# Optimization experiments

Measured on AMD Instinct MI355X. Metric: run time of the kernel, lower is better.

## Reference

```python
import jax, jax.numpy as jnp
from jax import lax
import numpy as np

B, P, N = 4, 12000, 100   # batch, max_pillars, max_points_per_pillar
H, W = 108, 124           # pseudo-image size from forward()
DN = ('NCHW', 'HWIO', 'NCHW')


def _conv(x, k, b):
    y = lax.conv_general_dilated(x, k, (1, 1), 'SAME', dimension_numbers=DN)
    return y + b[None, :, None, None]


def _cbr(x, k, b, s, t):
    # Conv2d + folded BatchNorm2d (eval: per-channel scale/shift) + ReLU
    y = _conv(x, k, b)
    return jax.nn.relu(y * s[None, :, None, None] + t[None, :, None, None])


def _pool(x):
    return lax.reduce_window(x, -jnp.inf, lax.max, (1, 1, 2, 2), (1, 1, 2, 2), 'VALID')


def setup_inputs() -> dict:
    key = jax.random.key(0)
    ks = iter(jax.random.split(key, 64))
    d = {}
    d['pillars'] = jax.random.normal(next(ks), (B, P, N, 9), jnp.float32)

    def w(shape, scale=0.05):
        return jax.random.normal(next(ks), shape, jnp.float32) * scale

    d['w1'] = w((9, 64)); d['b1'] = w((64,))
    d['s1'] = 1.0 + w((64,)); d['t1'] = w((64,))
    d['w2'] = w((64, 64)); d['b2'] = w((64,))
    d['s2'] = 1.0 + w((64,)); d['t2'] = w((64,))
    chans = [(64, 64), (64, 64), (64, 128), (128, 128), (128, 256), (256, 256)]
    for i, (ci, co) in enumerate(chans, 1):
        d['ck%d' % i] = w((3, 3, ci, co)); d['cb%d' % i] = w((co,))
        d['cs%d' % i] = 1.0 + w((co,)); d['ct%d' % i] = w((co,))
    d['hk1'] = w((3, 3, 256, 256)); d['hb1'] = w((256,))
    d['hk2'] = w((1, 1, 256, 10)); d['hb2'] = w((10,))
    d['num_points'] = jax.random.randint(next(ks), (B, P), 0, 100, jnp.int32)
    return d


def reference(pillars, w1, b1, s1, t1, w2, b2, s2, t2,
              ck1, cb1, cs1, ct1, ck2, cb2, cs2, ct2,
              ck3, cb3, cs3, ct3, ck4, cb4, cs4, ct4,
              ck5, cb5, cs5, ct5, ck6, cb6, cs6, ct6,
              hk1, hb1, hk2, hb2, num_points):
    # pillar feature net: Linear+BN(folded)+ReLU x2, batched over all points  [B,P,N,9] -> [B,P,N,64]
    h = jax.nn.relu((pillars @ w1 + b1) * s1 + t1)
    h = jax.nn.relu((h @ w2 + b2) * s2 + t2)
    # masked segment-max over the variable-length point groups
    mask = jnp.arange(N)[None, None, :] < num_points[:, :, None]          # [B,P,N]
    neg = jnp.finfo(h.dtype).min
    feat = jnp.max(jnp.where(mask[..., None], h, neg), axis=2)            # [B,P,64]
    valid = num_points > 0
    feat = jnp.where(valid[..., None], feat, 0.0)
    cnt = jnp.maximum(jnp.sum(valid, axis=1), 1).astype(feat.dtype)       # [B]
    mean = jnp.sum(feat, axis=1) / cnt[:, None]                           # [B,64]
    # nearest-interpolate a 1x1 map to HxW == broadcast
    x = jnp.broadcast_to(mean[:, :, None, None], (pillars.shape[0], 64, H, W))
    # 2D backbone
    x = _cbr(x, ck1, cb1, cs1, ct1); x = _cbr(x, ck2, cb2, cs2, ct2); x = _pool(x)
    x = _cbr(x, ck3, cb3, cs3, ct3); x = _cbr(x, ck4, cb4, cs4, ct4); x = _pool(x)
    x = _cbr(x, ck5, cb5, cs5, ct5); x = _cbr(x, ck6, cb6, cs6, ct6)
    # detection head
    y = jax.nn.relu(_conv(x, hk1, hb1))
    return _conv(y, hk2, hb2)   # [B, num_classes+7=10, 27, 31]
```

## Files before the change

### kernel.cpp

```cpp
#include <hip/hip_runtime.h>

typedef __bf16 vbf8 __attribute__((ext_vector_type(8)));
typedef __bf16 vbf4 __attribute__((ext_vector_type(4)));
typedef unsigned short us8 __attribute__((ext_vector_type(8)));
typedef float f32x4 __attribute__((ext_vector_type(4)));
typedef float f32x4u __attribute__((ext_vector_type(4), aligned(4)));

__global__ void setup_kernel(const float* __restrict__ w1, const float* __restrict__ b1,
                             const float* __restrict__ s1, const float* __restrict__ t1,
                             const float* __restrict__ w2, const float* __restrict__ b2,
                             const float* __restrict__ s2, const float* __restrict__ t2,
                             __bf16* __restrict__ wfrag, float4* __restrict__ cfrag) {
  int l = threadIdx.x;
  int s = l & 15, g = l >> 4;
#pragma unroll
  for (int n = 0; n < 4; ++n) {
    int co = s + 16 * n;
#pragma unroll
    for (int e = 0; e < 8; ++e) {
      int k = g * 8 + e;
      wfrag[(n * 64 + l) * 8 + e] = (k < 9) ? (__bf16)w1[k * 64 + co] : (__bf16)0.f;
      wfrag[((4 + n) * 64 + l) * 8 + e] = (__bf16)w2[k * 64 + co];
      wfrag[((8 + n) * 64 + l) * 8 + e] = (__bf16)w2[(32 + k) * 64 + co];
    }
    cfrag[n * 64 + l] = make_float4(s1[co], fmaf(b1[co], s1[co], t1[co]),
                                    s2[co], fmaf(b2[co], s2[co], t2[co]));
  }
}

__global__ void convw_kernel(const float* __restrict__ k1, const float* __restrict__ k2,
                             const float* __restrict__ k3, const float* __restrict__ k4,
                             const float* __restrict__ k5, const float* __restrict__ k6,
                             const float* __restrict__ kh, __bf16* __restrict__ wT) {
  int id = blockIdx.x * 256 + threadIdx.x;
  if (id >= 1769472) return;
  const float* src; int CI, CO, base;
  if (id < 36864)        { src = k1; base = 0;       CI = 64;  CO = 64; }
  else if (id < 73728)   { src = k2; base = 36864;   CI = 64;  CO = 64; }
  else if (id < 147456)  { src = k3; base = 73728;   CI = 64;  CO = 128; }
  else if (id < 294912)  { src = k4; base = 147456;  CI = 128; CO = 128; }
  else if (id < 589824)  { src = k5; base = 294912;  CI = 128; CO = 256; }
  else if (id < 1179648) { src = k6; base = 589824;  CI = 256; CO = 256; }
  else                   { src = kh; base = 1179648; CI = 256; CO = 256; }
  int loc = id - base;
  int tap = loc / (CI * CO); int rem = loc % (CI * CO);
  int co = rem / CI; int ci = rem % CI;
  wT[id] = (__bf16)src[(tap * CI + ci) * CO + co];
}

__global__ void zero_borders_kernel(__bf16* __restrict__ a64, __bf16* __restrict__ b64,
                                    __bf16* __restrict__ c128a, __bf16* __restrict__ c128b,
                                    __bf16* __restrict__ c256a, __bf16* __restrict__ c256b) {
  int idx = blockIdx.x * 256 + threadIdx.x;
  __bf16* buf; int H2, C, p;
  if (idx < 34848)       { buf = (idx < 17424) ? a64 : b64;     H2 = 66; C = 64;  p = idx % 17424; }
  else if (idx < 44096)  { int q = idx - 34848; buf = (q < 4624) ? c128a : c128b; H2 = 34; C = 128; p = q % 4624; }
  else if (idx < 46688)  { int q = idx - 44096; buf = (q < 1296) ? c256a : c256b; H2 = 18; C = 256; p = q % 1296; }
  else return;
  int w = p % H2; int h = (p / H2) % H2;
  if (h != 0 && h != H2 - 1 && w != 0 && w != H2 - 1) return;
  us8 zz = {0, 0, 0, 0, 0, 0, 0, 0};
  __bf16* q = buf + (size_t)p * C;
  for (int c = 0; c < C; c += 8) *(us8*)(q + c) = zz;
}

__global__ __launch_bounds__(256) void pillar_kernel(
    const float* __restrict__ pil, const int* __restrict__ npt,
    const __bf16* __restrict__ wfrag, const float4* __restrict__ cfrag,
    float* __restrict__ partial, int* __restrict__ pcnt)
{
  __shared__ __bf16 ldsa[4][16 * 80];
  __shared__ float redf[4][64];
  __shared__ int redc[4];
  const int tid = threadIdx.x;
  const int wv = tid >> 6, lane = tid & 63;
  const int s = lane & 15, g = lane >> 4;
  __bf16* lds = ldsa[wv];
  const int wid = blockIdx.x * 4 + wv;
  const int b = wid / 6000;
  const int p0 = (wid - b * 6000) * 2;

  vbf8 w1f[4], w2f0[4], w2f1[4];
  float a1[4], be1[4], a2[4], be2[4];
#pragma unroll
  for (int n = 0; n < 4; ++n) {
    w1f[n]  = *(const vbf8*)(wfrag + ((0 + n) * 64 + lane) * 8);
    w2f0[n] = *(const vbf8*)(wfrag + ((4 + n) * 64 + lane) * 8);
    w2f1[n] = *(const vbf8*)(wfrag + ((8 + n) * 64 + lane) * 8);
    float4 c = cfrag[n * 64 + lane];
    a1[n] = c.x; be1[n] = c.y; a2[n] = c.z; be2[n] = c.w;
  }

  float fsum[4] = {0.f, 0.f, 0.f, 0.f};
  int cnt = 0;

  for (int i = 0; i < 2; ++i) {
    int pidx = b * 12000 + p0 + i;
    int np = npt[pidx];
    if (np <= 0) continue;
    ++cnt;
    float feat[4][4];
#pragma unroll
    for (int n = 0; n < 4; ++n)
#pragma unroll
      for (int r = 0; r < 4; ++r) feat[n][r] = 0.f;

    int ngrp = (np + 15) >> 4;
    const float* pbase = pil + (size_t)pidx * 900;
    for (int grp = 0; grp < ngrp; ++grp) {
      int pt = grp * 16 + s; pt = min(pt, 99);
      const float* ptp = pbase + pt * 9;
      f32x4u lo = *(const f32x4u*)ptp;
      f32x4u hi = *(const f32x4u*)(ptp + 4);
      float v8 = ptp[8];
      vbf8 af;
      af[0] = (__bf16)(g == 0 ? lo[0] : (g == 1 ? v8 : 0.f));
      af[1] = (__bf16)(g == 0 ? lo[1] : 0.f);
      af[2] = (__bf16)(g == 0 ? lo[2] : 0.f);
      af[3] = (__bf16)(g == 0 ? lo[3] : 0.f);
      af[4] = (__bf16)(g == 0 ? hi[0] : 0.f);
      af[5] = (__bf16)(g == 0 ? hi[1] : 0.f);
      af[6] = (__bf16)(g == 0 ? hi[2] : 0.f);
      af[7] = (__bf16)(g == 0 ? hi[3] : 0.f);

      const f32x4 z = {0.f, 0.f, 0.f, 0.f};
      f32x4 d1[4];
#pragma unroll
      for (int n = 0; n < 4; ++n)
        d1[n] = __builtin_amdgcn_mfma_f32_16x16x32_bf16(af, w1f[n], z, 0, 0, 0);

#pragma unroll
      for (int n = 0; n < 4; ++n)
#pragma unroll
        for (int r = 0; r < 4; ++r) {
          float h = fmaxf(fmaf(d1[n][r], a1[n], be1[n]), 0.f);
          int pt2 = g * 4 + r;
          int ch = (s + 16 * n) ^ ((pt2 >> 2) << 3);
          lds[pt2 * 80 + ch] = (__bf16)h;
        }
      __builtin_amdgcn_wave_barrier();

      vbf8 a2f0 = *(const vbf8*)(lds + s * 80 + ((g * 8) ^ ((s >> 2) << 3)));
      vbf8 a2f1 = *(const vbf8*)(lds + s * 80 + ((32 + g * 8) ^ ((s >> 2) << 3)));
      f32x4 d2[4];
#pragma unroll
      for (int n = 0; n < 4; ++n) {
        d2[n] = __builtin_amdgcn_mfma_f32_16x16x32_bf16(a2f0, w2f0[n], z, 0, 0, 0);
        d2[n] = __builtin_amdgcn_mfma_f32_16x16x32_bf16(a2f1, w2f1[n], d2[n], 0, 0, 0);
      }
#pragma unroll
      for (int n = 0; n < 4; ++n)
#pragma unroll
        for (int r = 0; r < 4; ++r) {
          float h = fmaxf(fmaf(d2[n][r], a2[n], be2[n]), 0.f);
          if (grp * 16 + g * 4 + r < np) feat[n][r] = fmaxf(feat[n][r], h);
        }
    }
#pragma unroll
    for (int n = 0; n < 4; ++n) {
      float m = fmaxf(fmaxf(feat[n][0], feat[n][1]), fmaxf(feat[n][2], feat[n][3]));
      m = fmaxf(m, __shfl_xor(m, 16));
      m = fmaxf(m, __shfl_xor(m, 32));
      fsum[n] += m;
    }
  }
  if (g == 0) {
#pragma unroll
    for (int n = 0; n < 4; ++n) redf[wv][s + 16 * n] = fsum[n];
  }
  if (lane == 0) redc[wv] = cnt;
  __syncthreads();
  if (tid < 64) {
    float tot = redf[0][tid] + redf[1][tid] + redf[2][tid] + redf[3][tid];
    partial[blockIdx.x * 64 + tid] = tot;
    if (tid == 0) pcnt[blockIdx.x] = redc[0] + redc[1] + redc[2] + redc[3];
  }
}

__global__ void mean_kernel(const float* __restrict__ partial,
                            const int* __restrict__ pcnt,
                            float* __restrict__ mean) {
  int b = blockIdx.x, t = threadIdx.x;
  int c = t & 63, q = t >> 6;
  float sum = 0.f;
  for (int w = q; w < 1500; w += 4) sum += partial[(b * 1500 + w) * 64 + c];
  int cl = 0;
  for (int w = t; w < 1500; w += 256) cl += pcnt[b * 1500 + w];
  __shared__ float sh[256];
  __shared__ int shc[256];
  sh[t] = sum; shc[t] = cl;
  __syncthreads();
  for (int o = 128; o > 0; o >>= 1) {
    if (t < o) shc[t] += shc[t + o];
    __syncthreads();
  }
  if (t < 64) {
    float tot = sh[t] + sh[t + 64] + sh[t + 128] + sh[t + 192];
    mean[b * 64 + t] = tot / (float)(shc[0] > 0 ? shc[0] : 1);
  }
}

__global__ void broadcast_kernel(const float* __restrict__ mean,
                                 __bf16* __restrict__ x0) {
  int idx = blockIdx.x * 256 + threadIdx.x;
  int c8 = idx & 7; int rest = idx >> 3;
  int w = rest & 63; rest >>= 6;
  int h = rest & 63; int b = rest >> 6;
  const float* mb = mean + b * 64 + c8 * 8;
  vbf8 v;
#pragma unroll
  for (int e = 0; e < 8; ++e) v[e] = (__bf16)mb[e];
  *(vbf8*)(x0 + (((size_t)(b * 66 + h + 1) * 66) + (w + 1)) * 64 + c8 * 8) = v;
}

template <int CIN, int COUT, int HW>
__global__ __launch_bounds__(256) void kconv_kernel(
    const __bf16* __restrict__ x, const __bf16* __restrict__ wt,
    float* __restrict__ kpart)
{
  constexpr int H2 = HW + 2;
  constexpr int NT = COUT / 64;
  constexpr int KC = CIN / 32;
  constexpr int MTOT = 4 * HW * HW;
  constexpr int LOG = (HW == 64) ? 6 : (HW == 32) ? 5 : 4;
  const int tid = threadIdx.x, wv = tid >> 6, lane = tid & 63;
  const int s = lane & 15, g = lane >> 4;
  const int task = blockIdx.x * 4 + wv;
  const int kg = task % 3;
  const int t2 = task / 3;
  const int nt = t2 % NT;
  const int mt = t2 / NT;
  const int m0 = mt * 32;
  const int b = m0 >> (2 * LOG);
  const int mb = m0 - (b << (2 * LOG));

  size_t arow[2];
#pragma unroll
  for (int mf = 0; mf < 2; ++mf) {
    int m = mb + mf * 16 + s;
    int hh = m >> LOG, ww = m & (HW - 1);
    arow[mf] = ((size_t)(b * H2 + hh) * H2 + ww) * CIN;
  }

  f32x4 acc[2][4];
#pragma unroll
  for (int mf = 0; mf < 2; ++mf)
#pragma unroll
    for (int nf = 0; nf < 4; ++nf) acc[mf][nf] = (f32x4){0.f, 0.f, 0.f, 0.f};

#pragma unroll
  for (int j = 0; j < 3; ++j) {
    const int tap = kg * 3 + j;
    const int dh = tap / 3, dw = tap % 3;
    const size_t aoff = ((size_t)dh * H2 + dw) * CIN + 8 * g;
    const __bf16* wtap = wt + ((size_t)tap * COUT + nt * 64) * CIN + 8 * g;
#pragma unroll 2
    for (int ck = 0; ck < KC; ++ck) {
      vbf8 a0 = *(const vbf8*)(x + arow[0] + aoff + ck * 32);
      vbf8 a1 = *(const vbf8*)(x + arow[1] + aoff + ck * 32);
#pragma unroll
      for (int nf = 0; nf < 4; ++nf) {
        vbf8 bb = *(const vbf8*)(wtap + (size_t)(nf * 16 + s) * CIN + ck * 32);
        acc[0][nf] = __builtin_amdgcn_mfma_f32_16x16x32_bf16(a0, bb, acc[0][nf], 0, 0, 0);
        acc[1][nf] = __builtin_amdgcn_mfma_f32_16x16x32_bf16(a1, bb, acc[1][nf], 0, 0, 0);
      }
    }
  }

  float* kp = kpart + (size_t)kg * MTOT * COUT;
#pragma unroll
  for (int mf = 0; mf < 2; ++mf)
#pragma unroll
    for (int nf = 0; nf < 4; ++nf) {
      int co = nt * 64 + nf * 16 + s;
#pragma unroll
      for (int r = 0; r < 4; ++r) {
        int m = m0 + mf * 16 + 4 * g + r;
        kp[(size_t)m * COUT + co] = acc[mf][nf][r];
      }
    }
}

template <int COUT, int HW, bool HAS_BN, bool OUT_F32>
__global__ __launch_bounds__(256) void reduce_kernel(
    const float* __restrict__ kpart, const float* __restrict__ cb,
    const float* __restrict__ cs, const float* __restrict__ ct,
    __bf16* __restrict__ ypad, float* __restrict__ yf32)
{
  constexpr int H2 = HW + 2;
  constexpr int MTOT = 4 * HW * HW;
  constexpr int CQ = COUT / 4;
  constexpr int LOG = (HW == 64) ? 6 : (HW == 32) ? 5 : 4;
  int idx = blockIdx.x * 256 + threadIdx.x;
  int cq = idx % CQ; int m = idx / CQ;
  int co0 = cq * 4;
  const f32x4* f4 = (const f32x4*)kpart;
  f32x4 v = f4[(size_t)m * CQ + cq];
  f32x4 v1 = f4[((size_t)MTOT + m) * CQ + cq];
  f32x4 v2 = f4[((size_t)2 * MTOT + m) * CQ + cq];
  v += v1 + v2;
  f32x4 r;
  if (HAS_BN) {
    f32x4 sc = *(const f32x4*)(cs + co0);
    f32x4 bb = *(const f32x4*)(cb + co0);
    f32x4 tt = *(const f32x4*)(ct + co0);
#pragma unroll
    for (int e = 0; e < 4; ++e) r[e] = fmaxf(fmaf(v[e], sc[e], fmaf(bb[e], sc[e], tt[e])), 0.f);
  } else {
    f32x4 bb = *(const f32x4*)(cb + co0);
#pragma unroll
    for (int e = 0; e < 4; ++e) r[e] = fmaxf(v[e] + bb[e], 0.f);
  }
  if constexpr (OUT_F32) {
    *(f32x4*)(yf32 + (size_t)m * COUT + co0) = r;
  } else {
    int b = m >> (2 * LOG);
    int mm = m - (b << (2 * LOG));
    int hh = mm >> LOG, ww = mm & (HW - 1);
    vbf4 o;
#pragma unroll
    for (int e = 0; e < 4; ++e) o[e] = (__bf16)r[e];
    *(vbf4*)(ypad + (((size_t)(b * H2 + hh + 1) * H2) + ww + 1) * COUT + co0) = o;
  }
}

template <int C, int HI>
__global__ void pool_kernel(const __bf16* __restrict__ x, __bf16* __restrict__ y) {
  constexpr int HO = HI / 2, W2I = HI + 2, W2O = HO + 2, C8 = C / 8;
  int idx = blockIdx.x * 256 + threadIdx.x;
  if (idx >= 4 * W2O * W2O * C8) return;
  int c8 = idx % C8; int rest = idx / C8;
  int wo = rest % W2O; rest /= W2O;
  int ho = rest % W2O; int b = rest / W2O;
  us8 out;
  if (ho == 0 || ho == W2O - 1 || wo == 0 || wo == W2O - 1) {
    out = (us8){0, 0, 0, 0, 0, 0, 0, 0};
  } else {
    int hi = 2 * (ho - 1) + 1, wi = 2 * (wo - 1) + 1;
    const unsigned short* p =
        (const unsigned short*)x + (((size_t)(b * W2I + hi) * W2I) + wi) * C + c8 * 8;
    us8 v0 = *(const us8*)p;
    us8 v1 = *(const us8*)(p + C);
    us8 v2 = *(const us8*)(p + (size_t)W2I * C);
    us8 v3 = *(const us8*)(p + (size_t)W2I * C + C);
#pragma unroll
    for (int e = 0; e < 8; ++e) {
      unsigned short a = v0[e] > v1[e] ? v0[e] : v1[e];
      unsigned short c = v2[e] > v3[e] ? v2[e] : v3[e];
      out[e] = a > c ? a : c;
    }
  }
  *(us8*)((unsigned short*)y + (((size_t)(b * W2O + ho) * W2O) + wo) * C + c8 * 8) = out;
}

__global__ void head2_kernel(const float* __restrict__ x, const float* __restrict__ wk,
                             const float* __restrict__ bias, float* __restrict__ y) {
  int h = blockIdx.x, b = blockIdx.y;
  int t = threadIdx.x;
  int co = t & 15, w = t >> 4;
  if (co >= 10) return;
  const float* xr = x + ((size_t)(b * 16 + h) * 16 + w) * 256;
  float acc = 0.f;
#pragma unroll 4
  for (int ci = 0; ci < 256; ci += 4) {
    float4 in4 = *(const float4*)(xr + ci);
    acc = fmaf(in4.x, wk[(ci + 0) * 10 + co], acc);
    acc = fmaf(in4.y, wk[(ci + 1) * 10 + co], acc);
    acc = fmaf(in4.z, wk[(ci + 2) * 10 + co], acc);
    acc = fmaf(in4.w, wk[(ci + 3) * 10 + co], acc);
  }
  y[((size_t)(b * 16 + h) * 16 + w) * 10 + co] = acc + bias[co];
}

__global__ void scatter_kernel(const float* __restrict__ y, float* __restrict__ out) {
  int idx = blockIdx.x * 256 + threadIdx.x;
  if (idx >= 4 * 10 * 27 * 31) return;
  int c = idx % 31;
  int r = (idx / 31) % 27;
  int ch = (idx / (31 * 27)) % 10;
  int b = idx / (31 * 27 * 10);
  int rr = (r <= 7) ? r : ((r >= 20) ? r - 11 : 7);
  int cc = (c <= 7) ? c : ((c >= 24) ? c - 15 : 7);
  out[idx] = y[((size_t)(b * 16 + rr) * 16 + cc) * 10 + ch];
}

extern "C" void kernel_launch(void* const* d_in, const int* in_sizes, int n_in,
                              void* d_out, int out_size, void* d_ws, size_t ws_size,
                              hipStream_t stream) {
  (void)in_sizes; (void)n_in; (void)out_size; (void)ws_size;
  const float* pillars = (const float*)d_in[0];
  const float* w1 = (const float*)d_in[1];
  const float* b1 = (const float*)d_in[2];
  const float* s1 = (const float*)d_in[3];
  const float* t1 = (const float*)d_in[4];
  const float* w2 = (const float*)d_in[5];
  const float* b2 = (const float*)d_in[6];
  const float* s2 = (const float*)d_in[7];
  const float* t2 = (const float*)d_in[8];
  const float* ck[6], *cbv[6], *csv[6], *ctv[6];
  for (int i = 0; i < 6; ++i) {
    ck[i]  = (const float*)d_in[9 + i * 4];
    cbv[i] = (const float*)d_in[10 + i * 4];
    csv[i] = (const float*)d_in[11 + i * 4];
    ctv[i] = (const float*)d_in[12 + i * 4];
  }
  const float* hk1 = (const float*)d_in[33];
  const float* hb1 = (const float*)d_in[34];
  const float* hk2 = (const float*)d_in[35];
  const float* hb2 = (const float*)d_in[36];
  const int* num_points = (const int*)d_in[37];
  float* out = (float*)d_out;

  char* wsb = (char*)d_ws;
  size_t off = 0;
  auto alloc = [&](size_t n) { char* p = wsb + off; off = (off + n + 255) & ~(size_t)255; return p; };
  float*  kpart  = (float*)alloc(12582912);
  float*  ppart  = (float*)alloc(1536000);
  int*    pcnt   = (int*)alloc(24000);
  float*  mean   = (float*)alloc(1024);
  __bf16* wfrag  = (__bf16*)alloc(12288);
  float4* cfrag  = (float4*)alloc(4096);
  float*  h2out  = (float*)alloc(40960);
  __bf16* wT     = (__bf16*)alloc(3538944);
  __bf16* A64    = (__bf16*)alloc(2230272);
  __bf16* B64    = (__bf16*)alloc(2230272);
  __bf16* PL64   = (__bf16*)alloc(591872);
  __bf16* C128A  = (__bf16*)alloc(1183744);
  __bf16* C128B  = (__bf16*)alloc(1183744);
  __bf16* PL128  = (__bf16*)alloc(331776);
  __bf16* C256A  = (__bf16*)alloc(663552);
  __bf16* C256B  = (__bf16*)alloc(663552);
  float*  h1out  = (float*)alloc(1048576);

  __bf16* wt1 = wT + 0;       __bf16* wt2 = wT + 36864;
  __bf16* wt3 = wT + 73728;   __bf16* wt4 = wT + 147456;
  __bf16* wt5 = wT + 294912;  __bf16* wt6 = wT + 589824;
  __bf16* wth = wT + 1179648;

  setup_kernel<<<1, 64, 0, stream>>>(w1, b1, s1, t1, w2, b2, s2, t2, wfrag, cfrag);
  convw_kernel<<<6912, 256, 0, stream>>>(ck[0], ck[1], ck[2], ck[3], ck[4], ck[5],
                                         hk1, wT);
  zero_borders_kernel<<<183, 256, 0, stream>>>(A64, B64, C128A, C128B, C256A, C256B);

  pillar_kernel<<<6000, 256, 0, stream>>>(pillars, num_points, wfrag, cfrag,
                                          ppart, pcnt);
  mean_kernel<<<4, 256, 0, stream>>>(ppart, pcnt, mean);
  broadcast_kernel<<<512, 256, 0, stream>>>(mean, A64);

  kconv_kernel<64, 64, 64><<<384, 256, 0, stream>>>(A64, wt1, kpart);
  reduce_kernel<64, 64, true, false><<<1024, 256, 0, stream>>>(
      kpart, cbv[0], csv[0], ctv[0], B64, nullptr);
  kconv_kernel<64, 64, 64><<<384, 256, 0, stream>>>(B64, wt2, kpart);
  reduce_kernel<64, 64, true, false><<<1024, 256, 0, stream>>>(
      kpart, cbv[1], csv[1], ctv[1], A64, nullptr);
  pool_kernel<64, 64><<<145, 256, 0, stream>>>(A64, PL64);
  kconv_kernel<64, 128, 32><<<192, 256, 0, stream>>>(PL64, wt3, kpart);
  reduce_kernel<128, 32, true, false><<<512, 256, 0, stream>>>(
      kpart, cbv[2], csv[2], ctv[2], C128A, nullptr);
  kconv_kernel<128, 128, 32><<<192, 256, 0, stream>>>(C128A, wt4, kpart);
  reduce_kernel<128, 32, true, false><<<512, 256, 0, stream>>>(
      kpart, cbv[3], csv[3], ctv[3], C128B, nullptr);
  pool_kernel<128, 32><<<81, 256, 0, stream>>>(C128B, PL128);
  kconv_kernel<128, 256, 16><<<96, 256, 0, stream>>>(PL128, wt5, kpart);
  reduce_kernel<256, 16, true, false><<<256, 256, 0, stream>>>(
      kpart, cbv[4], csv[4], ctv[4], C256A, nullptr);
  kconv_kernel<256, 256, 16><<<96, 256, 0, stream>>>(C256A, wt6, kpart);
  reduce_kernel<256, 16, true, false><<<256, 256, 0, stream>>>(
      kpart, cbv[5], csv[5], ctv[5], C256B, nullptr);
  kconv_kernel<256, 256, 16><<<96, 256, 0, stream>>>(C256B, wth, kpart);
  reduce_kernel<256, 16, false, true><<<256, 256, 0, stream>>>(
      kpart, hb1, nullptr, nullptr, nullptr, h1out);

  head2_kernel<<<dim3(16, 4), 256, 0, stream>>>(h1out, hk2, hb2, h2out);
  scatter_kernel<<<131, 256, 0, stream>>>(h2out, out);
}
```

Baseline: 372.3 us.

## Fold BN into pillar MLP weights, keep layer-1 output in registers, tile weight transpose

The first-layer MFMA is transposed so its output lands directly in the A-fragment layout for the second layer, removing the LDS round-trip and wave barrier. BatchNorm scale is folded into the bf16 weights, and the layer-1 bias rides as an extra K column of constant 1. The layer-2 shift is fed as the MFMA accumulator init. Full groups skip the per-point mask, and the conv-weight transpose now goes through a shared-memory tile for coalesced accesses. The cost is slightly different bf16 rounding from folding the scales into the weights.

Result: faster. 340.8 us (-8.5%).

```diff
diff --git a/kernel.cpp b/kernel.cpp
--- a/kernel.cpp
+++ b/kernel.cpp
@@ -10,42 +10,64 @@
                              const float* __restrict__ s1, const float* __restrict__ t1,
                              const float* __restrict__ w2, const float* __restrict__ b2,
                              const float* __restrict__ s2, const float* __restrict__ t2,
-                             __bf16* __restrict__ wfrag, float4* __restrict__ cfrag) {
+                             __bf16* __restrict__ wfrag, float* __restrict__ be2f) {
   int l = threadIdx.x;
   int s = l & 15, g = l >> 4;
 #pragma unroll
-  for (int n = 0; n < 4; ++n) {
-    int co = s + 16 * n;
+  for (int m = 0; m < 4; ++m) {
+    int c = 32 * (m & 1) + 8 * (s >> 2) + 4 * (m >> 1) + (s & 3);
 #pragma unroll
     for (int e = 0; e < 8; ++e) {
       int k = g * 8 + e;
-      wfrag[(n * 64 + l) * 8 + e] = (k < 9) ? (__bf16)w1[k * 64 + co] : (__bf16)0.f;
-      wfrag[((4 + n) * 64 + l) * 8 + e] = (__bf16)w2[k * 64 + co];
-      wfrag[((8 + n) * 64 + l) * 8 + e] = (__bf16)w2[(32 + k) * 64 + co];
-    }
-    cfrag[n * 64 + l] = make_float4(s1[co], fmaf(b1[co], s1[co], t1[co]),
-                                    s2[co], fmaf(b2[co], s2[co], t2[co]));
-  }
-}
-
-__global__ void convw_kernel(const float* __restrict__ k1, const float* __restrict__ k2,
-                             const float* __restrict__ k3, const float* __restrict__ k4,
-                             const float* __restrict__ k5, const float* __restrict__ k6,
-                             const float* __restrict__ kh, __bf16* __restrict__ wT) {
-  int id = blockIdx.x * 256 + threadIdx.x;
-  if (id >= 1769472) return;
-  const float* src; int CI, CO, base;
-  if (id < 36864)        { src = k1; base = 0;       CI = 64;  CO = 64; }
-  else if (id < 73728)   { src = k2; base = 36864;   CI = 64;  CO = 64; }
-  else if (id < 147456)  { src = k3; base = 73728;   CI = 64;  CO = 128; }
-  else if (id < 294912)  { src = k4; base = 147456;  CI = 128; CO = 128; }
-  else if (id < 589824)  { src = k5; base = 294912;  CI = 128; CO = 256; }
-  else if (id < 1179648) { src = k6; base = 589824;  CI = 256; CO = 256; }
-  else                   { src = kh; base = 1179648; CI = 256; CO = 256; }
-  int loc = id - base;
-  int tap = loc / (CI * CO); int rem = loc % (CI * CO);
-  int co = rem / CI; int ci = rem % CI;
-  wT[id] = (__bf16)src[(tap * CI + ci) * CO + co];
+      float v = 0.f;
+      if (k < 9)       v = w1[k * 64 + c] * s1[c];
+      else if (k == 9) v = fmaf(b1[c], s1[c], t1[c]);
+      wfrag[(m * 64 + l) * 8 + e] = (__bf16)v;
+    }
+    int co = s + 16 * m;
+#pragma unroll
+    for (int e = 0; e < 8; ++e) {
+      int k = g * 8 + e;
+      wfrag[((4 + m) * 64 + l) * 8 + e] = (__bf16)(w2[k * 64 + co] * s2[co]);
+      wfrag[((8 + m) * 64 + l) * 8 + e] = (__bf16)(w2[(32 + k) * 64 + co] * s2[co]);
+    }
+    be2f[m * 64 + l] = fmaf(b2[co], s2[co], t2[co]);
+  }
+}
+
+__global__ __launch_bounds__(256) void convw_kernel(
+    const float* __restrict__ k1, const float* __restrict__ k2,
+    const float* __restrict__ k3, const float* __restrict__ k4,
+    const float* __restrict__ k5, const float* __restrict__ k6,
+    const float* __restrict__ kh, __bf16* __restrict__ wT) {
+  __shared__ float tile[64][65];
+  const int tCI[7]    = {64, 64, 64, 128, 128, 256, 256};
+  const int tCO[7]    = {64, 64, 128, 128, 256, 256, 256};
+  const int tOFF[7]   = {0, 36864, 73728, 147456, 294912, 589824, 1179648};
+  const int tTILES[7] = {9, 9, 18, 36, 72, 144, 144};
+  int bid = blockIdx.x;
+  int ti = 0, acc = 0;
+  while (ti < 6 && bid >= acc + tTILES[ti]) { acc += tTILES[ti]; ++ti; }
+  int lt = bid - acc;
+  int CI = tCI[ti], CO = tCO[ti];
+  const float* src;
+  if (ti == 0) src = k1; else if (ti == 1) src = k2; else if (ti == 2) src = k3;
+  else if (ti == 3) src = k4; else if (ti == 4) src = k5; else if (ti == 5) src = k6;
+  else src = kh;
+  int cot = CO / 64, tpt = (CI / 64) * cot;
+  int tap = lt / tpt; int r2 = lt - tap * tpt;
+  int ci0 = (r2 / cot) * 64, co0 = (r2 % cot) * 64;
+  const float* sp = src + (size_t)(tap * CI + ci0) * CO + co0;
+  int t = threadIdx.x;
+  int lr = t >> 6, lc = t & 63;
+#pragma unroll
+  for (int rr = 0; rr < 64; rr += 4)
+    tile[rr + lr][lc] = sp[(size_t)(rr + lr) * CO + lc];
+  __syncthreads();
+  __bf16* dst = wT + tOFF[ti] + ((size_t)tap * CO + co0) * CI + ci0;
+#pragma unroll
+  for (int rr = 0; rr < 64; rr += 4)
+    dst[(size_t)(rr + lr) * CI + lc] = (__bf16)tile[lc][rr + lr];
 }
 
 __global__ void zero_borders_kernel(__bf16* __restrict__ a64, __bf16* __restrict__ b64,
@@ -66,29 +88,26 @@
 
 __global__ __launch_bounds__(256) void pillar_kernel(
     const float* __restrict__ pil, const int* __restrict__ npt,
-    const __bf16* __restrict__ wfrag, const float4* __restrict__ cfrag,
+    const __bf16* __restrict__ wfrag, const float* __restrict__ be2f,
     float* __restrict__ partial, int* __restrict__ pcnt)
 {
-  __shared__ __bf16 ldsa[4][16 * 80];
   __shared__ float redf[4][64];
   __shared__ int redc[4];
   const int tid = threadIdx.x;
   const int wv = tid >> 6, lane = tid & 63;
   const int s = lane & 15, g = lane >> 4;
-  __bf16* lds = ldsa[wv];
   const int wid = blockIdx.x * 4 + wv;
   const int b = wid / 6000;
   const int p0 = (wid - b * 6000) * 2;
 
   vbf8 w1f[4], w2f0[4], w2f1[4];
-  float a1[4], be1[4], a2[4], be2[4];
-#pragma unroll
-  for (int n = 0; n < 4; ++n) {
-    w1f[n]  = *(const vbf8*)(wfrag + ((0 + n) * 64 + lane) * 8);
-    w2f0[n] = *(const vbf8*)(wfrag + ((4 + n) * 64 + lane) * 8);
-    w2f1[n] = *(const vbf8*)(wfrag + ((8 + n) * 64 + lane) * 8);
-    float4 c = cfrag[n * 64 + lane];
-    a1[n] = c.x; be1[n] = c.y; a2[n] = c.z; be2[n] = c.w;
+  float be2[4];
+#pragma unroll
+  for (int m = 0; m < 4; ++m) {
+    w1f[m]  = *(const vbf8*)(wfrag + ((0 + m) * 64 + lane) * 8);
+    w2f0[m] = *(const vbf8*)(wfrag + ((4 + m) * 64 + lane) * 8);
+    w2f1[m] = *(const vbf8*)(wfrag + ((8 + m) * 64 + lane) * 8);
+    be2[m] = be2f[m * 64 + lane];
   }
 
   float fsum[4] = {0.f, 0.f, 0.f, 0.f};
@@ -113,48 +132,52 @@
       f32x4u lo = *(const f32x4u*)ptp;
       f32x4u hi = *(const f32x4u*)(ptp + 4);
       float v8 = ptp[8];
-      vbf8 af;
-      af[0] = (__bf16)(g == 0 ? lo[0] : (g == 1 ? v8 : 0.f));
-      af[1] = (__bf16)(g == 0 ? lo[1] : 0.f);
-      af[2] = (__bf16)(g == 0 ? lo[2] : 0.f);
-      af[3] = (__bf16)(g == 0 ? lo[3] : 0.f);
-      af[4] = (__bf16)(g == 0 ? hi[0] : 0.f);
-      af[5] = (__bf16)(g == 0 ? hi[1] : 0.f);
-      af[6] = (__bf16)(g == 0 ? hi[2] : 0.f);
-      af[7] = (__bf16)(g == 0 ? hi[3] : 0.f);
+      vbf8 b1f;
+      b1f[0] = (__bf16)(g == 0 ? lo[0] : (g == 1 ? v8 : 0.f));
+      b1f[1] = (__bf16)(g == 0 ? lo[1] : (g == 1 ? 1.0f : 0.f));
+      b1f[2] = (__bf16)(g == 0 ? lo[2] : 0.f);
+      b1f[3] = (__bf16)(g == 0 ? lo[3] : 0.f);
+      b1f[4] = (__bf16)(g == 0 ? hi[0] : 0.f);
+      b1f[5] = (__bf16)(g == 0 ? hi[1] : 0.f);
+      b1f[6] = (__bf16)(g == 0 ? hi[2] : 0.f);
+      b1f[7] = (__bf16)(g == 0 ? hi[3] : 0.f);
 
       const f32x4 z = {0.f, 0.f, 0.f, 0.f};
       f32x4 d1[4];
 #pragma unroll
-      for (int n = 0; n < 4; ++n)
-        d1[n] = __builtin_amdgcn_mfma_f32_16x16x32_bf16(af, w1f[n], z, 0, 0, 0);
-
-#pragma unroll
-      for (int n = 0; n < 4; ++n)
-#pragma unroll
-        for (int r = 0; r < 4; ++r) {
-          float h = fmaxf(fmaf(d1[n][r], a1[n], be1[n]), 0.f);
-          int pt2 = g * 4 + r;
-          int ch = (s + 16 * n) ^ ((pt2 >> 2) << 3);
-          lds[pt2 * 80 + ch] = (__bf16)h;
-        }
-      __builtin_amdgcn_wave_barrier();
-
-      vbf8 a2f0 = *(const vbf8*)(lds + s * 80 + ((g * 8) ^ ((s >> 2) << 3)));
-      vbf8 a2f1 = *(const vbf8*)(lds + s * 80 + ((32 + g * 8) ^ ((s >> 2) << 3)));
+      for (int m = 0; m < 4; ++m)
+        d1[m] = __builtin_amdgcn_mfma_f32_16x16x32_bf16(w1f[m], b1f, z, 0, 0, 0);
+
+      vbf8 a2f0, a2f1;
+#pragma unroll
+      for (int r = 0; r < 4; ++r) {
+        a2f0[r]     = (__bf16)fmaxf(d1[0][r], 0.f);
+        a2f1[r]     = (__bf16)fmaxf(d1[1][r], 0.f);
+        a2f0[4 + r] = (__bf16)fmaxf(d1[2][r], 0.f);
+        a2f1[4 + r] = (__bf16)fmaxf(d1[3][r], 0.f);
+      }
+
       f32x4 d2[4];
 #pragma unroll
       for (int n = 0; n < 4; ++n) {
-        d2[n] = __builtin_amdgcn_mfma_f32_16x16x32_bf16(a2f0, w2f0[n], z, 0, 0, 0);
+        f32x4 cb = {be2[n], be2[n], be2[n], be2[n]};
+        d2[n] = __builtin_amdgcn_mfma_f32_16x16x32_bf16(a2f0, w2f0[n], cb, 0, 0, 0);
         d2[n] = __builtin_amdgcn_mfma_f32_16x16x32_bf16(a2f1, w2f1[n], d2[n], 0, 0, 0);
       }
-#pragma unroll
-      for (int n = 0; n < 4; ++n)
-#pragma unroll
-        for (int r = 0; r < 4; ++r) {
-          float h = fmaxf(fmaf(d2[n][r], a2[n], be2[n]), 0.f);
-          if (grp * 16 + g * 4 + r < np) feat[n][r] = fmaxf(feat[n][r], h);
-        }
+      if (((grp + 1) << 4) <= np) {
+#pragma unroll
+        for (int n = 0; n < 4; ++n)
+#pragma unroll
+          for (int r = 0; r < 4; ++r) feat[n][r] = fmaxf(feat[n][r], d2[n][r]);
+      } else {
+#pragma unroll
+        for (int n = 0; n < 4; ++n)
+#pragma unroll
+          for (int r = 0; r < 4; ++r) {
+            float vv = (grp * 16 + 4 * g + r < np) ? d2[n][r] : 0.f;
+            feat[n][r] = fmaxf(feat[n][r], vv);
+          }
+      }
     }
 #pragma unroll
     for (int n = 0; n < 4; ++n) {
@@ -419,7 +442,7 @@
   int*    pcnt   = (int*)alloc(24000);
   float*  mean   = (float*)alloc(1024);
   __bf16* wfrag  = (__bf16*)alloc(12288);
-  float4* cfrag  = (float4*)alloc(4096);
+  float*  be2f   = (float*)alloc(1024);
   float*  h2out  = (float*)alloc(40960);
   __bf16* wT     = (__bf16*)alloc(3538944);
   __bf16* A64    = (__bf16*)alloc(2230272);
@@ -437,12 +460,12 @@
   __bf16* wt5 = wT + 294912;  __bf16* wt6 = wT + 589824;
   __bf16* wth = wT + 1179648;
 
-  setup_kernel<<<1, 64, 0, stream>>>(w1, b1, s1, t1, w2, b2, s2, t2, wfrag, cfrag);
-  convw_kernel<<<6912, 256, 0, stream>>>(ck[0], ck[1], ck[2], ck[3], ck[4], ck[5],
-                                         hk1, wT);
+  setup_kernel<<<1, 64, 0, stream>>>(w1, b1, s1, t1, w2, b2, s2, t2, wfrag, be2f);
+  convw_kernel<<<432, 256, 0, stream>>>(ck[0], ck[1], ck[2], ck[3], ck[4], ck[5],
+                                        hk1, wT);
   zero_borders_kernel<<<183, 256, 0, stream>>>(A64, B64, C128A, C128B, C256A, C256B);
 
-  pillar_kernel<<<6000, 256, 0, stream>>>(pillars, num_points, wfrag, cfrag,
+  pillar_kernel<<<6000, 256, 0, stream>>>(pillars, num_points, wfrag, be2f,
                                           ppart, pcnt);
   mean_kernel<<<4, 256, 0, stream>>>(ppart, pcnt, mean);
   broadcast_kernel<<<512, 256, 0, stream>>>(mean, A64);
```
